# Kernel optimization log

Hardware: AMD Instinct MI355X
Metric: run time of the kernel (lower is better)

Reference implementation:

```python
import jax, jax.numpy as jnp
import numpy as np

GAMMA0 = 1.0


def patch_to_image(patches):
    # patches: [b, n_patch, patch_dim, 1, T] -> image [b, 1, g*p, g*p, T]
    b, n_patch, patch_dim, _, T = patches.shape
    p = int(patch_dim ** 0.5)
    g = int(n_patch ** 0.5)
    img = patches[:, :, :, 0, :]                      # [b, n_patch, p*p, T]
    img = jnp.transpose(img, (0, 3, 1, 2))            # [b, T, n_patch, p*p]
    img = img.reshape(b, T, g, g, p, p)
    img = jnp.transpose(img, (0, 1, 2, 4, 3, 5)).reshape(b, T, 1, g * p, g * p)
    return jnp.transpose(img, (0, 2, 3, 4, 1))        # [b, 1, g*p, g*p, T]


def setup_inputs() -> dict:
    key = jax.random.key(0)
    k0, k1, k2, k3, k4, k5 = jax.random.split(key, 6)
    X = jax.random.normal(k0, (32, 64, 300, 1, 50), dtype=jnp.float32)
    U = jax.random.normal(k1, (32, 1, 40, 1, 50), dtype=jnp.float32)
    x0 = jax.random.normal(k2, (32, 64, 300, 1), dtype=jnp.float32)
    # dictionaries, column-normalized like torch's norm(dim=2, keepdim=True)
    A = jax.random.uniform(k3, (300, 300), dtype=jnp.float32)
    A = A / jnp.linalg.norm(A, axis=0, keepdims=True)
    B = jax.random.uniform(k4, (300, 40), dtype=jnp.float32)
    B = B / jnp.linalg.norm(B, axis=0, keepdims=True)
    C = jax.random.uniform(k5, (256, 300), dtype=jnp.float32)
    C = C / jnp.linalg.norm(C, axis=0, keepdims=True)
    return {"X": X, "U": U, "x0": x0, "A": A, "B": B, "C": C}


def reference(X, U, x0, A, B, C):
    # X: [b, P, 300, 1, T]  U: [b, 1, 40, 1, T]  x0: [b, P, 300, 1]
    # Prediction x_hat_t = A @ x_{t-1}, with x_{-1} = x0 (vectorized over T)
    x_prev = jnp.concatenate([x0[..., None], X[..., :-1]], axis=-1)   # [b,P,300,1,T]
    X_pred = jnp.einsum('ij,bpjut->bpiut', A, x_prev)                 # [b,P,300,1,T]
    # Reconstruction recon_t = C @ x_t, assembled into frames
    recon = jnp.einsum('dj,bpjut->bpdut', C, X)                       # [b,P,256,1,T]
    vid_recon = patch_to_image(recon)                                 # [b,1,128,128,T]
    # Cause state: gamma_t * sum_patches |x_t|
    Bu = jnp.einsum('ij,bqjut->bqiut', B, U)                          # [b,1,300,1,T]
    gamma = GAMMA0 * (1.0 + jnp.exp(-Bu)) / 2.0
    X_U = gamma * jnp.sum(jnp.abs(X), axis=1, keepdims=True)          # [b,1,300,1,T]
    return (vid_recon, X_pred, X_U)
```

## Files before the change

kernel.cpp:

```cpp
#include <hip/hip_runtime.h>

typedef _Float16 half8 __attribute__((ext_vector_type(8)));
typedef _Float16 half4v __attribute__((ext_vector_type(4)));
typedef float f32x4 __attribute__((ext_vector_type(4)));
typedef unsigned long long ull;

#define OFF_PRED 26214400
#define OFF_XU   56934400

__global__ void build_M(const float* __restrict__ A, const float* __restrict__ C,
                        _Float16* __restrict__ M) {
    int idx = blockIdx.x * 256 + threadIdx.x;
    if (idx >= 640 * 320) return;
    int e    = idx & 7;
    int lane = (idx >> 3) & 63;
    int fs   = idx >> 9;
    int mt = fs / 10, ks = fs % 10;
    int m = mt * 16 + (lane & 15);
    int k = ks * 32 + (lane >> 4) * 8 + e;
    float v = 0.f;
    if (k < 300) {
        if (m < 256) v = C[m * 300 + k];
        else if (m < 556) v = A[(m - 256) * 300 + k];
    }
    M[idx] = (_Float16)v;
}

__global__ __launch_bounds__(256, 3) void gemm_main(
    const float* __restrict__ X, const float* __restrict__ x0,
    const _Float16* __restrict__ M, float* __restrict__ out)
{
    __shared__ _Float16 lds[64 * 320];
    char* ldsb = (char*)lds;
    const int orig = ((blockIdx.x & 7) << 9) + (blockIdx.x >> 3);
    const int bp = orig >> 1, mhalf = orig & 1;
    const int b = bp >> 6, p = bp & 63;
    const int tid = threadIdx.x;
    const float* Xbp = X + bp * 15000;

    const int wave = tid >> 6, lane = tid & 63;
    const int lr = lane & 15, lg = lane >> 4;
    const int g = wave;

    const _Float16* Mw = M + (mhalf * 4 + g) * 50 * 512 + lane * 8;

    half8 pf[5];
    #pragma unroll
    for (int j = 0; j < 5; j++) pf[j] = *(const half8*)(Mw + (j * 10) * 512);

    if (tid < 255) {
        int row = tid / 5, c = tid % 5;
        *(ull*)(ldsb + row * 640 + ((600 + c * 8) ^ ((row & 7) << 4))) = 0ULL;
    }
    #pragma unroll
    for (int u = 0; u < 5; u++) {
        int i = tid + u * 256;
        if (i < 1040) *(ull*)(ldsb + 51 * 640 + i * 8) = 0ULL;
    }
    if (tid < 75) {
        f32x4 v = *(const f32x4*)(x0 + bp * 300 + tid * 4);
        half4v h4 = { (_Float16)v.x, (_Float16)v.y, (_Float16)v.z, (_Float16)v.w };
        *(half4v*)(ldsb + tid * 8) = h4;
    }
    #pragma unroll
    for (int u = 0; u < 8; u++) {
        int i = tid + u * 256;
        if (i < 1875) {
            int tp = i % 25, jq = i / 25;
            const float* s = Xbp + jq * 200 + tp * 2;
            float2 v0 = *(const float2*)(s);
            float2 v1 = *(const float2*)(s + 50);
            float2 v2 = *(const float2*)(s + 100);
            float2 v3 = *(const float2*)(s + 150);
            int r1 = tp * 2 + 1, r2 = tp * 2 + 2;
            half4v h1 = { (_Float16)v0.x, (_Float16)v1.x, (_Float16)v2.x, (_Float16)v3.x };
            half4v h2 = { (_Float16)v0.y, (_Float16)v1.y, (_Float16)v2.y, (_Float16)v3.y };
            *(half4v*)(ldsb + r1 * 640 + ((jq * 8) ^ ((r1 & 7) << 4))) = h1;
            *(half4v*)(ldsb + r2 * 640 + ((jq * 8) ^ ((r2 & 7) << 4))) = h2;
        }
    }
    __syncthreads();

    f32x4 acc[5][4];
    #pragma unroll
    for (int j = 0; j < 5; j++)
        #pragma unroll
        for (int nt = 0; nt < 4; nt++)
            acc[j][nt] = (f32x4){0.f, 0.f, 0.f, 0.f};

    #define LDSA(nt, ks) (*(const half8*)(ldsb + ((nt) * 16 + lr) * 640 + \
                         (((ks) * 64 + lg * 16) ^ ((lr & 7) << 4))))

    #pragma unroll
    for (int ks = 0; ks < 10; ks++) {
        half8 bf0, bf1, bf2, bf3, bf4;
        if (ks == 0) {
            bf0 = pf[0]; bf1 = pf[1]; bf2 = pf[2]; bf3 = pf[3]; bf4 = pf[4];
        } else {
            bf0 = *(const half8*)(Mw + (0 * 10 + ks) * 512);
            bf1 = *(const half8*)(Mw + (1 * 10 + ks) * 512);
            bf2 = *(const half8*)(Mw + (2 * 10 + ks) * 512);
            bf3 = *(const half8*)(Mw + (3 * 10 + ks) * 512);
            bf4 = *(const half8*)(Mw + (4 * 10 + ks) * 512);
        }
        #pragma unroll
        for (int nt = 0; nt < 4; nt++) {
            half8 a = LDSA(nt, ks);
            acc[0][nt] = __builtin_amdgcn_mfma_f32_16x16x32_f16(a, bf0, acc[0][nt], 0, 0, 0);
            acc[1][nt] = __builtin_amdgcn_mfma_f32_16x16x32_f16(a, bf1, acc[1][nt], 0, 0, 0);
            acc[2][nt] = __builtin_amdgcn_mfma_f32_16x16x32_f16(a, bf2, acc[2][nt], 0, 0, 0);
            acc[3][nt] = __builtin_amdgcn_mfma_f32_16x16x32_f16(a, bf3, acc[3][nt], 0, 0, 0);
            acc[4][nt] = __builtin_amdgcn_mfma_f32_16x16x32_f16(a, bf4, acc[4][nt], 0, 0, 0);
        }
    }

    const int gr = p >> 3, gc = p & 7;
    #pragma unroll
    for (int j = 0; j < 5; j++) {
        int colm = mhalf * 320 + g * 80 + j * 16 + lr;
        if (colm < 256) {
            int base = b * 819200 + ((gr * 16 + (colm >> 4)) * 128 + gc * 16 + (colm & 15)) * 50;
            #pragma unroll
            for (int nt = 0; nt < 4; nt++) {
                int t0 = nt * 16 + lg * 4;
                if (t0 == 0) {
                    out[base + 0] = acc[j][0][1];
                    out[base + 1] = acc[j][0][2];
                    out[base + 2] = acc[j][0][3];
                } else if (t0 <= 46) {
                    f32x4 v = acc[j][nt];
                    __builtin_memcpy(&out[base + t0 - 1], &v, 16);
                } else if (t0 == 48) {
                    out[base + 47] = acc[j][nt][0];
                    out[base + 48] = acc[j][nt][1];
                    out[base + 49] = acc[j][nt][2];
                }
            }
        } else if (colm < 556) {
            int base = OFF_PRED + (bp * 300 + (colm - 256)) * 50;
            #pragma unroll
            for (int nt = 0; nt < 4; nt++) {
                int t0 = nt * 16 + lg * 4;
                if (t0 <= 46) {
                    f32x4 v = acc[j][nt];
                    __builtin_memcpy(&out[base + t0], &v, 16);
                } else if (t0 == 48) {
                    out[base + 48] = acc[j][nt][0];
                    out[base + 49] = acc[j][nt][1];
                }
            }
        }
    }
    #undef LDSA
}

__global__ void xu_kernel(const float* __restrict__ X, const float* __restrict__ U,
                          const float* __restrict__ B, float* __restrict__ out) {
    int id = blockIdx.x * 256 + threadIdx.x;
    if (id >= 480000) return;
    int t = id % 50;
    int i = (id / 50) % 300;
    int b = id / 15000;
    const float* xp = X + b * 960000 + i * 50 + t;
    float s = 0.f;
    #pragma unroll 8
    for (int pp = 0; pp < 64; pp++) s += fabsf(xp[pp * 15000]);
    float bu = 0.f;
    const float* up = U + b * 2000 + t;
    const float* Bp = B + i * 40;
    #pragma unroll 8
    for (int q = 0; q < 40; q++) bu += Bp[q] * up[q * 50];
    out[OFF_XU + id] = 0.5f * (1.f + expf(-bu)) * s;
}

extern "C" void kernel_launch(void* const* d_in, const int* in_sizes, int n_in,
                              void* d_out, int out_size, void* d_ws, size_t ws_size,
                              hipStream_t stream) {
    const float* X  = (const float*)d_in[0];
    const float* U  = (const float*)d_in[1];
    const float* x0 = (const float*)d_in[2];
    const float* A  = (const float*)d_in[3];
    const float* B  = (const float*)d_in[4];
    const float* C  = (const float*)d_in[5];
    float* out = (float*)d_out;
    _Float16* M = (_Float16*)d_ws;

    build_M<<<800, 256, 0, stream>>>(A, C, M);
    gemm_main<<<4096, 256, 0, stream>>>(X, x0, M, out);
    xu_kernel<<<1875, 256, 0, stream>>>(X, U, B, out);
}
```

Before: 134.1 us.

## Process two patches per block to reuse dictionary fragments across GEMM tiles

Result: faster. 125.1 us (-6.7%).

```diff
diff --git a/kernel.cpp b/kernel.cpp
--- a/kernel.cpp
+++ b/kernel.cpp
@@ -26,17 +26,16 @@
     M[idx] = (_Float16)v;
 }
 
-__global__ __launch_bounds__(256, 3) void gemm_main(
+__global__ __launch_bounds__(256, 2) void gemm_main(
     const float* __restrict__ X, const float* __restrict__ x0,
     const _Float16* __restrict__ M, float* __restrict__ out)
 {
-    __shared__ _Float16 lds[64 * 320];
+    __shared__ _Float16 lds[2 * 64 * 320];
     char* ldsb = (char*)lds;
-    const int orig = ((blockIdx.x & 7) << 9) + (blockIdx.x >> 3);
-    const int bp = orig >> 1, mhalf = orig & 1;
-    const int b = bp >> 6, p = bp & 63;
+    const int sw = ((blockIdx.x & 7) << 8) + (blockIdx.x >> 3);
+    const int bpp = sw >> 1, mhalf = sw & 1;
+    const int bp0 = bpp * 2;
     const int tid = threadIdx.x;
-    const float* Xbp = X + bp * 15000;
 
     const int wave = tid >> 6, lane = tid & 63;
     const int lr = lane & 15, lg = lane >> 4;
@@ -48,48 +47,57 @@
     #pragma unroll
     for (int j = 0; j < 5; j++) pf[j] = *(const half8*)(Mw + (j * 10) * 512);
 
-    if (tid < 255) {
-        int row = tid / 5, c = tid % 5;
-        *(ull*)(ldsb + row * 640 + ((600 + c * 8) ^ ((row & 7) << 4))) = 0ULL;
-    }
-    #pragma unroll
-    for (int u = 0; u < 5; u++) {
+    #pragma unroll
+    for (int tau = 0; tau < 2; tau++) {
+        char* lb = ldsb + tau * 40960;
+        if (tid < 255) {
+            int row = tid / 5, c = tid % 5;
+            *(ull*)(lb + row * 640 + ((600 + c * 8) ^ ((row & 7) << 4))) = 0ULL;
+        }
+        #pragma unroll
+        for (int u = 0; u < 5; u++) {
+            int i = tid + u * 256;
+            if (i < 1040) *(ull*)(lb + 51 * 640 + i * 8) = 0ULL;
+        }
+    }
+    if (tid < 150) {
+        int tau = tid / 75, c = tid - tau * 75;
+        f32x4 v = *(const f32x4*)(x0 + (bp0 + tau) * 300 + c * 4);
+        half4v h4 = { (_Float16)v.x, (_Float16)v.y, (_Float16)v.z, (_Float16)v.w };
+        *(half4v*)(ldsb + tau * 40960 + c * 8) = h4;
+    }
+    #pragma unroll
+    for (int u = 0; u < 15; u++) {
         int i = tid + u * 256;
-        if (i < 1040) *(ull*)(ldsb + 51 * 640 + i * 8) = 0ULL;
-    }
-    if (tid < 75) {
-        f32x4 v = *(const f32x4*)(x0 + bp * 300 + tid * 4);
-        half4v h4 = { (_Float16)v.x, (_Float16)v.y, (_Float16)v.z, (_Float16)v.w };
-        *(half4v*)(ldsb + tid * 8) = h4;
-    }
-    #pragma unroll
-    for (int u = 0; u < 8; u++) {
-        int i = tid + u * 256;
-        if (i < 1875) {
-            int tp = i % 25, jq = i / 25;
-            const float* s = Xbp + jq * 200 + tp * 2;
+        if (i < 3750) {
+            int tau = i / 1875, rem = i - tau * 1875;
+            int tp = rem % 25, jq = rem / 25;
+            const float* s = X + (bp0 + tau) * 15000 + jq * 200 + tp * 2;
             float2 v0 = *(const float2*)(s);
             float2 v1 = *(const float2*)(s + 50);
             float2 v2 = *(const float2*)(s + 100);
             float2 v3 = *(const float2*)(s + 150);
+            char* lb = ldsb + tau * 40960;
             int r1 = tp * 2 + 1, r2 = tp * 2 + 2;
             half4v h1 = { (_Float16)v0.x, (_Float16)v1.x, (_Float16)v2.x, (_Float16)v3.x };
             half4v h2 = { (_Float16)v0.y, (_Float16)v1.y, (_Float16)v2.y, (_Float16)v3.y };
-            *(half4v*)(ldsb + r1 * 640 + ((jq * 8) ^ ((r1 & 7) << 4))) = h1;
-            *(half4v*)(ldsb + r2 * 640 + ((jq * 8) ^ ((r2 & 7) << 4))) = h2;
+            *(half4v*)(lb + r1 * 640 + ((jq * 8) ^ ((r1 & 7) << 4))) = h1;
+            *(half4v*)(lb + r2 * 640 + ((jq * 8) ^ ((r2 & 7) << 4))) = h2;
         }
     }
     __syncthreads();
 
-    f32x4 acc[5][4];
+    f32x4 acc0[5][4], acc1[5][4];
     #pragma unroll
     for (int j = 0; j < 5; j++)
         #pragma unroll
-        for (int nt = 0; nt < 4; nt++)
-            acc[j][nt] = (f32x4){0.f, 0.f, 0.f, 0.f};
-
-    #define LDSA(nt, ks) (*(const half8*)(ldsb + ((nt) * 16 + lr) * 640 + \
-                         (((ks) * 64 + lg * 16) ^ ((lr & 7) << 4))))
+        for (int nt = 0; nt < 4; nt++) {
+            acc0[j][nt] = (f32x4){0.f, 0.f, 0.f, 0.f};
+            acc1[j][nt] = (f32x4){0.f, 0.f, 0.f, 0.f};
+        }
+
+    #define LDSA(TB, nt, ks) (*(const half8*)(ldsb + (TB) + ((nt) * 16 + lr) * 640 + \
+                             (((ks) * 64 + lg * 16) ^ ((lr & 7) << 4))))
 
     #pragma unroll
     for (int ks = 0; ks < 10; ks++) {
@@ -105,53 +113,68 @@
         }
         #pragma unroll
         for (int nt = 0; nt < 4; nt++) {
-            half8 a = LDSA(nt, ks);
-            acc[0][nt] = __builtin_amdgcn_mfma_f32_16x16x32_f16(a, bf0, acc[0][nt], 0, 0, 0);
-            acc[1][nt] = __builtin_amdgcn_mfma_f32_16x16x32_f16(a, bf1, acc[1][nt], 0, 0, 0);
-            acc[2][nt] = __builtin_amdgcn_mfma_f32_16x16x32_f16(a, bf2, acc[2][nt], 0, 0, 0);
-            acc[3][nt] = __builtin_amdgcn_mfma_f32_16x16x32_f16(a, bf3, acc[3][nt], 0, 0, 0);
-            acc[4][nt] = __builtin_amdgcn_mfma_f32_16x16x32_f16(a, bf4, acc[4][nt], 0, 0, 0);
-        }
-    }
-
-    const int gr = p >> 3, gc = p & 7;
-    #pragma unroll
-    for (int j = 0; j < 5; j++) {
-        int colm = mhalf * 320 + g * 80 + j * 16 + lr;
-        if (colm < 256) {
-            int base = b * 819200 + ((gr * 16 + (colm >> 4)) * 128 + gc * 16 + (colm & 15)) * 50;
-            #pragma unroll
-            for (int nt = 0; nt < 4; nt++) {
-                int t0 = nt * 16 + lg * 4;
-                if (t0 == 0) {
-                    out[base + 0] = acc[j][0][1];
-                    out[base + 1] = acc[j][0][2];
-                    out[base + 2] = acc[j][0][3];
-                } else if (t0 <= 46) {
-                    f32x4 v = acc[j][nt];
-                    __builtin_memcpy(&out[base + t0 - 1], &v, 16);
-                } else if (t0 == 48) {
-                    out[base + 47] = acc[j][nt][0];
-                    out[base + 48] = acc[j][nt][1];
-                    out[base + 49] = acc[j][nt][2];
-                }
-            }
-        } else if (colm < 556) {
-            int base = OFF_PRED + (bp * 300 + (colm - 256)) * 50;
-            #pragma unroll
-            for (int nt = 0; nt < 4; nt++) {
-                int t0 = nt * 16 + lg * 4;
-                if (t0 <= 46) {
-                    f32x4 v = acc[j][nt];
-                    __builtin_memcpy(&out[base + t0], &v, 16);
-                } else if (t0 == 48) {
-                    out[base + 48] = acc[j][nt][0];
-                    out[base + 49] = acc[j][nt][1];
-                }
-            }
+            half8 a = LDSA(0, nt, ks);
+            acc0[0][nt] = __builtin_amdgcn_mfma_f32_16x16x32_f16(a, bf0, acc0[0][nt], 0, 0, 0);
+            acc0[1][nt] = __builtin_amdgcn_mfma_f32_16x16x32_f16(a, bf1, acc0[1][nt], 0, 0, 0);
+            acc0[2][nt] = __builtin_amdgcn_mfma_f32_16x16x32_f16(a, bf2, acc0[2][nt], 0, 0, 0);
+            acc0[3][nt] = __builtin_amdgcn_mfma_f32_16x16x32_f16(a, bf3, acc0[3][nt], 0, 0, 0);
+            acc0[4][nt] = __builtin_amdgcn_mfma_f32_16x16x32_f16(a, bf4, acc0[4][nt], 0, 0, 0);
+        }
+        #pragma unroll
+        for (int nt = 0; nt < 4; nt++) {
+            half8 a = LDSA(40960, nt, ks);
+            acc1[0][nt] = __builtin_amdgcn_mfma_f32_16x16x32_f16(a, bf0, acc1[0][nt], 0, 0, 0);
+            acc1[1][nt] = __builtin_amdgcn_mfma_f32_16x16x32_f16(a, bf1, acc1[1][nt], 0, 0, 0);
+            acc1[2][nt] = __builtin_amdgcn_mfma_f32_16x16x32_f16(a, bf2, acc1[2][nt], 0, 0, 0);
+            acc1[3][nt] = __builtin_amdgcn_mfma_f32_16x16x32_f16(a, bf3, acc1[3][nt], 0, 0, 0);
+            acc1[4][nt] = __builtin_amdgcn_mfma_f32_16x16x32_f16(a, bf4, acc1[4][nt], 0, 0, 0);
         }
     }
     #undef LDSA
+
+#define EPILOGUE(ACC, BP) { \
+    const int b_ = (BP) >> 6, p_ = (BP) & 63; \
+    const int gr_ = p_ >> 3, gc_ = p_ & 7; \
+    _Pragma("unroll") \
+    for (int j = 0; j < 5; j++) { \
+        int colm = mhalf * 320 + g * 80 + j * 16 + lr; \
+        if (colm < 256) { \
+            int base = b_ * 819200 + ((gr_ * 16 + (colm >> 4)) * 128 + gc_ * 16 + (colm & 15)) * 50; \
+            _Pragma("unroll") \
+            for (int nt = 0; nt < 4; nt++) { \
+                int t0 = nt * 16 + lg * 4; \
+                if (t0 == 0) { \
+                    out[base + 0] = ACC[j][0][1]; \
+                    out[base + 1] = ACC[j][0][2]; \
+                    out[base + 2] = ACC[j][0][3]; \
+                } else if (t0 <= 46) { \
+                    f32x4 v = ACC[j][nt]; \
+                    __builtin_memcpy(&out[base + t0 - 1], &v, 16); \
+                } else if (t0 == 48) { \
+                    out[base + 47] = ACC[j][nt][0]; \
+                    out[base + 48] = ACC[j][nt][1]; \
+                    out[base + 49] = ACC[j][nt][2]; \
+                } \
+            } \
+        } else if (colm < 556) { \
+            int base = OFF_PRED + ((BP) * 300 + (colm - 256)) * 50; \
+            _Pragma("unroll") \
+            for (int nt = 0; nt < 4; nt++) { \
+                int t0 = nt * 16 + lg * 4; \
+                if (t0 <= 46) { \
+                    f32x4 v = ACC[j][nt]; \
+                    __builtin_memcpy(&out[base + t0], &v, 16); \
+                } else if (t0 == 48) { \
+                    out[base + 48] = ACC[j][nt][0]; \
+                    out[base + 49] = ACC[j][nt][1]; \
+                } \
+            } \
+        } \
+    } }
+
+    EPILOGUE(acc0, bp0);
+    EPILOGUE(acc1, bp0 + 1);
+#undef EPILOGUE
 }
 
 __global__ void xu_kernel(const float* __restrict__ X, const float* __restrict__ U,
@@ -186,6 +209,6 @@
     _Float16* M = (_Float16*)d_ws;
 
     build_M<<<800, 256, 0, stream>>>(A, C, M);
-    gemm_main<<<4096, 256, 0, stream>>>(X, x0, M, out);
+    gemm_main<<<2048, 256, 0, stream>>>(X, x0, M, out);
     xu_kernel<<<1875, 256, 0, stream>>>(X, U, B, out);
 }
```
